# Performance work log

Measured on AMD Instinct MI355X. Metric: run time of the kernel, lower is better.

Reference implementation:

```python
import jax, jax.numpy as jnp
import numpy as np

M = 1024       # input feature dim
T_EXPERTS = 64 # number of experts
K = 2          # top-k
TOKENS = 65536 # B*N flattened tokens


def setup_inputs() -> dict:
    key = jax.random.key(0)
    ks = jax.random.split(key, 6)
    return {
        "x": jax.random.normal(ks[0], (TOKENS, M), dtype=jnp.float32),
        "noise": jax.random.normal(ks[1], (TOKENS, T_EXPERTS), dtype=jnp.float32),
        "Wg_w": jax.random.normal(ks[2], (T_EXPERTS, M), dtype=jnp.float32) * 0.02,
        "Wg_b": jax.random.normal(ks[3], (T_EXPERTS,), dtype=jnp.float32) * 0.02,
        "Wn_w": jax.random.normal(ks[4], (T_EXPERTS, M), dtype=jnp.float32) * 0.02,
        "Wn_b": jax.random.normal(ks[5], (T_EXPERTS,), dtype=jnp.float32) * 0.02,
    }


def reference(x, noise, Wg_w, Wg_b, Wn_w, Wn_b):
    # logits = Wg(x); noise_scale = softplus(Wnoise(x))
    logits = jnp.einsum("bm,tm->bt", x, Wg_w) + Wg_b          # [tokens, t]
    noise_scale = jax.nn.softplus(jnp.einsum("bm,tm->bt", x, Wn_w) + Wn_b)
    H = logits + noise * noise_scale                           # noisy logits
    topk_vals, topk_idx = jax.lax.top_k(H, K)                  # [tokens, k]
    topk_softmax = jax.nn.softmax(topk_vals, axis=-1)
    # scatter softmax weights into sparse [tokens, t] gate tensor
    rows = jnp.arange(H.shape[0])[:, None]
    gates = jnp.zeros_like(H).at[rows, topk_idx].set(topk_softmax)
    return (gates, H, topk_idx, noise_scale, logits)
```

## Files before the change

kernel.cpp:

```cpp
#include <hip/hip_runtime.h>
#include <math.h>

#define NTOK 65536
#define MDIM 1024
#define NE   64
#define TB   128
#define NKC  32
#define DELTA 5e-4f

typedef float f32x4  __attribute__((ext_vector_type(4)));
typedef short bf16x8 __attribute__((ext_vector_type(8)));
typedef unsigned int u32;

__device__ __forceinline__ unsigned short f32_to_bf16_rne(float f) {
    u32 u = __builtin_bit_cast(u32, f);
    u32 r = u + 0x7FFFu + ((u >> 16) & 1u);
    return (unsigned short)(r >> 16);
}
__device__ __forceinline__ float bf16_to_f32(unsigned short h) {
    u32 u = ((u32)h) << 16;
    return __builtin_bit_cast(float, u);
}
__device__ __forceinline__ void gll16(const void* g, void* l) {
    __builtin_amdgcn_global_load_lds(
        (const __attribute__((address_space(1))) u32*)g,
        (__attribute__((address_space(3))) u32*)l, 16, 0, 0);
}

__global__ __launch_bounds__(256) void split_w_kernel(
    const float* __restrict__ Wg_w, const float* __restrict__ Wn_w,
    unsigned short* __restrict__ ws, u32* __restrict__ cnt)
{
    if (blockIdx.x == 0 && threadIdx.x == 0) *cnt = 0;

    const int gid  = blockIdx.x * 256 + threadIdx.x;
    const int kc   = gid >> 10;
    const int rest = gid & 1023;
    const int tm   = rest >> 8;
    const int mat  = (rest >> 7) & 1;
    const int sp   = (rest >> 6) & 1;
    const int lane = rest & 63;
    const int e    = (lane & 15) + 16 * tm;
    const int k0   = kc * 32 + 8 * (lane >> 4);
    const float* W = mat ? Wn_w : Wg_w;

    unsigned short o[8];
#pragma unroll
    for (int i = 0; i < 8; ++i) {
        const float v = W[(size_t)e * MDIM + k0 + i];
        const u32 u  = __builtin_bit_cast(u32, v);
        const unsigned short hb = (unsigned short)(u >> 16);
        o[i] = sp ? f32_to_bf16_rne(v - bf16_to_f32(hb)) : hb;
    }
    uint4 pk;
    pk.x = (u32)o[0] | ((u32)o[1] << 16);
    pk.y = (u32)o[2] | ((u32)o[3] << 16);
    pk.z = (u32)o[4] | ((u32)o[5] << 16);
    pk.w = (u32)o[6] | ((u32)o[7] << 16);
    *reinterpret_cast<uint4*>(&ws[(size_t)gid * 8]) = pk;
}

__global__ __launch_bounds__(512, 4) void gate_mfma_kernel(
    const float* __restrict__ x,
    const float* __restrict__ noise,
    const unsigned short* __restrict__ ws,
    const float* __restrict__ Wg_b,
    const float* __restrict__ Wn_b,
    float* __restrict__ out_gates,
    float* __restrict__ out_H,
    float* __restrict__ out_idx,
    float* __restrict__ out_ns,
    float* __restrict__ out_logits,
    u32* __restrict__ cnt,
    u32* __restrict__ list)
{
    __shared__ unsigned short wbuf[2][8192];

    const int tid  = threadIdx.x;
    const int lane = tid & 63;
    const int w    = tid >> 6;
    const int c    = lane & 15;
    const int q    = lane >> 4;
    const int tokw = blockIdx.x * TB + w * 16;

    const float* __restrict__ xr = x + (size_t)(tokw + c) * MDIM + 8 * q;

    f32x4 acc[4][2];
#pragma unroll
    for (int tm = 0; tm < 4; ++tm)
#pragma unroll
        for (int m = 0; m < 2; ++m)
            acc[tm][m] = (f32x4){0.f, 0.f, 0.f, 0.f};

    gll16(ws + (size_t)tid * 8,         &wbuf[0][(size_t)tid * 8]);
    gll16(ws + (size_t)(tid + 512) * 8, &wbuf[0][(size_t)(tid + 512) * 8]);
    __builtin_amdgcn_sched_barrier(0);
    f32x4 xa = *reinterpret_cast<const f32x4*>(xr);
    f32x4 xb = *reinterpret_cast<const f32x4*>(xr + 4);
    __builtin_amdgcn_sched_barrier(0);
    asm volatile("s_waitcnt vmcnt(2)" ::: "memory");
    __syncthreads();

    int cur = 0;
    for (int kc = 0; kc < NKC; ++kc) {
        asm volatile("s_waitcnt vmcnt(0)" ::: "memory");

        bf16x8 xhi, xlo;
        {
            const float v[8] = {xa.x, xa.y, xa.z, xa.w, xb.x, xb.y, xb.z, xb.w};
            u32 hp[4], lp[4];
#pragma unroll
            for (int p = 0; p < 4; ++p) {
                const u32 u0 = __builtin_bit_cast(u32, v[2 * p]);
                const u32 u1 = __builtin_bit_cast(u32, v[2 * p + 1]);
                const float h0 = __builtin_bit_cast(float, u0 & 0xFFFF0000u);
                const float h1 = __builtin_bit_cast(float, u1 & 0xFFFF0000u);
                hp[p] = (u0 >> 16) | (u1 & 0xFFFF0000u);
                const u32 l0 = (u32)f32_to_bf16_rne(v[2 * p] - h0);
                const u32 l1 = (u32)f32_to_bf16_rne(v[2 * p + 1] - h1);
                lp[p] = l0 | (l1 << 16);
            }
            const uint4 h4 = {hp[0], hp[1], hp[2], hp[3]};
            const uint4 l4 = {lp[0], lp[1], lp[2], lp[3]};
            xhi = __builtin_bit_cast(bf16x8, h4);
            xlo = __builtin_bit_cast(bf16x8, l4);
        }

        if (kc + 1 < NKC) {
            const unsigned short* wc = ws + (size_t)(kc + 1) * 8192;
            gll16(wc + (size_t)tid * 8,         &wbuf[cur ^ 1][(size_t)tid * 8]);
            gll16(wc + (size_t)(tid + 512) * 8, &wbuf[cur ^ 1][(size_t)(tid + 512) * 8]);
            __builtin_amdgcn_sched_barrier(0);
            const int off = (kc + 1) * 32;
            xa = *reinterpret_cast<const f32x4*>(xr + off);
            xb = *reinterpret_cast<const f32x4*>(xr + off + 4);
            __builtin_amdgcn_sched_barrier(0);
        }

#pragma unroll
        for (int tm = 0; tm < 4; ++tm)
#pragma unroll
            for (int mat = 0; mat < 2; ++mat) {
                const int gbase = ((tm * 4 + mat * 2) * 64 + lane) * 8;
                const bf16x8 whi = *reinterpret_cast<const bf16x8*>(&wbuf[cur][gbase]);
                const bf16x8 wlo = *reinterpret_cast<const bf16x8*>(&wbuf[cur][gbase + 512]);
                f32x4 a = acc[tm][mat];
                a = __builtin_amdgcn_mfma_f32_16x16x32_bf16(wlo, xhi, a, 0, 0, 0);
                a = __builtin_amdgcn_mfma_f32_16x16x32_bf16(whi, xlo, a, 0, 0, 0);
                a = __builtin_amdgcn_mfma_f32_16x16x32_bf16(whi, xhi, a, 0, 0, 0);
                acc[tm][mat] = a;
            }

        if (kc + 1 < NKC) {
            asm volatile("s_waitcnt vmcnt(2)" ::: "memory");
            __syncthreads();
        }
        cur ^= 1;
    }

    f32x4 bgv[4], bnv[4];
#pragma unroll
    for (int tm = 0; tm < 4; ++tm) {
        bgv[tm] = *reinterpret_cast<const f32x4*>(&Wg_b[16 * tm + 4 * q]);
        bnv[tm] = *reinterpret_cast<const f32x4*>(&Wn_b[16 * tm + 4 * q]);
    }

    const int tok = tokw + c;
    float hv[4][4];

#pragma unroll
    for (int tm = 0; tm < 4; ++tm) {
        const size_t rb = (size_t)tok * NE + 16 * tm + 4 * q;
        const f32x4 nz = *reinterpret_cast<const f32x4*>(&noise[rb]);
        f32x4 lg, nsv, hh;
#pragma unroll
        for (int r = 0; r < 4; ++r) {
            lg[r] = acc[tm][0][r] + bgv[tm][r];
            const float nl = acc[tm][1][r] + bnv[tm][r];
            nsv[r] = fmaxf(nl, 0.f) + log1pf(expf(-fabsf(nl)));
            hh[r]  = fmaf(nz[r], nsv[r], lg[r]);
            hv[tm][r] = hh[r];
        }
        *reinterpret_cast<f32x4*>(&out_logits[rb]) = lg;
        *reinterpret_cast<f32x4*>(&out_ns[rb])     = nsv;
        *reinterpret_cast<f32x4*>(&out_H[rb])      = hh;
    }

    float v1 = -INFINITY, v2 = -INFINITY, v3 = -INFINITY;
    int   i1 = 0,         i2 = 0;
#pragma unroll
    for (int tm = 0; tm < 4; ++tm)
#pragma unroll
        for (int r = 0; r < 4; ++r) {
            const int ex = 16 * tm + 4 * q + r;
            const float hcur = hv[tm][r];
            if (hcur > v1)      { v3 = v2; v2 = v1; i2 = i1; v1 = hcur; i1 = ex; }
            else if (hcur > v2) { v3 = v2; v2 = hcur; i2 = ex; }
            else if (hcur > v3) { v3 = hcur; }
        }

#pragma unroll
    for (int off = 16; off <= 32; off <<= 1) {
        const float w1 = __shfl_xor(v1, off, 64);
        const int   k1 = __shfl_xor(i1, off, 64);
        const float w2 = __shfl_xor(v2, off, 64);
        const int   k2 = __shfl_xor(i2, off, 64);
        const float w3 = __shfl_xor(v3, off, 64);
        float m3;
        if (v1 >= w1) m3 = (v2 >= w1) ? fmaxf(v3, w1) : fmaxf(v2, w2);
        else          m3 = (w2 >= v1) ? fmaxf(w3, v1) : fmaxf(w2, v2);
        if (w1 > v1 || (w1 == v1 && k1 < i1)) {
            if (v1 > w2 || (v1 == w2 && i1 < k2)) { v2 = v1; i2 = i1; }
            else                                  { v2 = w2; i2 = k2; }
            v1 = w1; i1 = k1;
        } else {
            if (w1 > v2 || (w1 == v2 && k1 < i2)) { v2 = w1; i2 = k1; }
        }
        v3 = m3;
    }

    const float e2v = expf(v2 - v1);
    const float inv = 1.f / (1.f + e2v);
    const float p1  = inv;
    const float p2  = e2v * inv;

#pragma unroll
    for (int tm = 0; tm < 4; ++tm) {
        f32x4 g;
#pragma unroll
        for (int r = 0; r < 4; ++r) {
            const int ex = 16 * tm + 4 * q + r;
            g[r] = (ex == i1) ? p1 : ((ex == i2) ? p2 : 0.f);
        }
        *reinterpret_cast<f32x4*>(&out_gates[(size_t)tok * NE + 16 * tm + 4 * q]) = g;
    }
    if (q == 0) {
        *reinterpret_cast<float2*>(&out_idx[(size_t)tok * 2]) =
            make_float2((float)i1, (float)i2);
        if ((v1 - v2 < DELTA) || (v2 - v3 < DELTA)) {
            const u32 slot = atomicAdd(cnt, 1u);
            list[slot] = (u32)tok;
        }
    }
}

__global__ __launch_bounds__(64) void refine_kernel(
    const float* __restrict__ x,
    const float* __restrict__ noise,
    const float* __restrict__ Wg_w, const float* __restrict__ Wg_b,
    const float* __restrict__ Wn_w, const float* __restrict__ Wn_b,
    const u32* __restrict__ cnt, const u32* __restrict__ list,
    float* __restrict__ out_gates, float* __restrict__ out_idx)
{
    const int lane = threadIdx.x;
    const u32 n = *cnt;

    for (u32 it = blockIdx.x; it < n; it += gridDim.x) {
        const int tok = (int)list[it];

        f32x4 xv[4];
#pragma unroll
        for (int i = 0; i < 4; ++i)
            xv[i] = *reinterpret_cast<const f32x4*>(
                &x[(size_t)tok * MDIM + lane * 16 + i * 4]);

        float lgv = 0.f, nlv = 0.f;
        for (int e = 0; e < NE; ++e) {
            float sg = 0.f, sn = 0.f;
#pragma unroll
            for (int i = 0; i < 4; ++i) {
                const f32x4 wg = *reinterpret_cast<const f32x4*>(
                    &Wg_w[(size_t)e * MDIM + lane * 16 + i * 4]);
                const f32x4 wn = *reinterpret_cast<const f32x4*>(
                    &Wn_w[(size_t)e * MDIM + lane * 16 + i * 4]);
#pragma unroll
                for (int j = 0; j < 4; ++j) {
                    sg = fmaf(xv[i][j], wg[j], sg);
                    sn = fmaf(xv[i][j], wn[j], sn);
                }
            }
#pragma unroll
            for (int off = 32; off >= 1; off >>= 1) {
                sg += __shfl_xor(sg, off, 64);
                sn += __shfl_xor(sn, off, 64);
            }
            if (e == lane) { lgv = sg; nlv = sn; }
        }

        lgv += Wg_b[lane];
        nlv += Wn_b[lane];
        const float ns = fmaxf(nlv, 0.f) + log1pf(expf(-fabsf(nlv)));
        const float h  = fmaf(noise[(size_t)tok * NE + lane], ns, lgv);

        float v1 = h; int i1 = lane;
#pragma unroll
        for (int off = 32; off >= 1; off >>= 1) {
            const float ov = __shfl_xor(v1, off, 64);
            const int   oi = __shfl_xor(i1, off, 64);
            if (ov > v1 || (ov == v1 && oi < i1)) { v1 = ov; i1 = oi; }
        }
        float v2 = (lane == i1) ? -INFINITY : h; int i2 = lane;
#pragma unroll
        for (int off = 32; off >= 1; off >>= 1) {
            const float ov = __shfl_xor(v2, off, 64);
            const int   oi = __shfl_xor(i2, off, 64);
            if (ov > v2 || (ov == v2 && oi < i2)) { v2 = ov; i2 = oi; }
        }

        const float e2v = expf(v2 - v1);
        const float inv = 1.f / (1.f + e2v);
        const float p1  = inv;
        const float p2  = e2v * inv;

        out_gates[(size_t)tok * NE + lane] =
            (lane == i1) ? p1 : ((lane == i2) ? p2 : 0.f);
        if (lane == 0) {
            *reinterpret_cast<float2*>(&out_idx[(size_t)tok * 2]) =
                make_float2((float)i1, (float)i2);
        }
    }
}

extern "C" void kernel_launch(void* const* d_in, const int* in_sizes, int n_in,
                              void* d_out, int out_size, void* d_ws, size_t ws_size,
                              hipStream_t stream) {
    const float* x     = (const float*)d_in[0];
    const float* noise = (const float*)d_in[1];
    const float* Wg_w  = (const float*)d_in[2];
    const float* Wg_b  = (const float*)d_in[3];
    const float* Wn_w  = (const float*)d_in[4];
    const float* Wn_b  = (const float*)d_in[5];

    float* out = (float*)d_out;
    float* out_gates  = out;
    float* out_H      = out + (size_t)NTOK * NE;
    float* out_idx    = out + (size_t)2 * NTOK * NE;
    float* out_ns     = out + (size_t)2 * NTOK * NE + (size_t)NTOK * 2;
    float* out_logits = out + (size_t)3 * NTOK * NE + (size_t)NTOK * 2;

    unsigned short* wsplit = (unsigned short*)d_ws;
    u32* cnt  = (u32*)((char*)d_ws + 524288);
    u32* list = (u32*)((char*)d_ws + 524304);

    split_w_kernel<<<dim3(128), dim3(256), 0, stream>>>(Wg_w, Wn_w, wsplit, cnt);
    gate_mfma_kernel<<<dim3(NTOK / TB), dim3(512), 0, stream>>>(
        x, noise, wsplit, Wg_b, Wn_b,
        out_gates, out_H, out_idx, out_ns, out_logits, cnt, list);
    refine_kernel<<<dim3(1024), dim3(64), 0, stream>>>(
        x, noise, Wg_w, Wg_b, Wn_w, Wn_b, cnt, list, out_gates, out_idx);
}
```

Measured before the change: 143.6 us.

## Prefetch x two chunks ahead and stagger K-chunk start per block

Restructures the K loop so x is loaded in bursts of two chunks, held in a double-buffered register set two groups ahead, and the loop is fully unrolled. Each block starts its K traversal at a different chunk offset, derived from the block index, so concurrent blocks spread their weight-chunk reads. The loop now waits only on the weight loads and lets the x loads run deeper in flight, aiming to hide HBM latency for the memory-bound x stream. It costs more VGPRs for the extra x buffers and a larger unrolled code body, and changes the fp32 accumulation order.

```diff
diff --git a/kernel.cpp b/kernel.cpp
--- a/kernel.cpp
+++ b/kernel.cpp
@@ -82,6 +82,7 @@
     const int c    = lane & 15;
     const int q    = lane >> 4;
     const int tokw = blockIdx.x * TB + w * 16;
+    const int p    = (blockIdx.x & 15) * 2;
 
     const float* __restrict__ xr = x + (size_t)(tokw + c) * MDIM + 8 * q;
 
@@ -92,71 +93,101 @@
         for (int m = 0; m < 2; ++m)
             acc[tm][m] = (f32x4){0.f, 0.f, 0.f, 0.f};
 
-    gll16(ws + (size_t)tid * 8,         &wbuf[0][(size_t)tid * 8]);
-    gll16(ws + (size_t)(tid + 512) * 8, &wbuf[0][(size_t)(tid + 512) * 8]);
-    __builtin_amdgcn_sched_barrier(0);
-    f32x4 xa = *reinterpret_cast<const f32x4*>(xr);
-    f32x4 xb = *reinterpret_cast<const f32x4*>(xr + 4);
-    __builtin_amdgcn_sched_barrier(0);
-    asm volatile("s_waitcnt vmcnt(2)" ::: "memory");
+    f32x4 xs[2][2][2];
+
+#define XBURST(G, SET)                                                          \
+    {                                                                           \
+        const int cA_ = (p + 2 * (G)) & (NKC - 1);                              \
+        const int cB_ = (p + 2 * (G) + 1) & (NKC - 1);                          \
+        xs[SET][0][0] = *reinterpret_cast<const f32x4*>(xr + cA_ * 32);         \
+        xs[SET][0][1] = *reinterpret_cast<const f32x4*>(xr + cA_ * 32 + 4);     \
+        xs[SET][1][0] = *reinterpret_cast<const f32x4*>(xr + cB_ * 32);         \
+        xs[SET][1][1] = *reinterpret_cast<const f32x4*>(xr + cB_ * 32 + 4);     \
+        __builtin_amdgcn_sched_barrier(0);                                      \
+    }
+#define WGLL(CI, BUF)                                                           \
+    {                                                                           \
+        const unsigned short* wc_ = ws + (size_t)(CI) * 8192;                   \
+        gll16(wc_ + (size_t)tid * 8,         &wbuf[BUF][(size_t)tid * 8]);      \
+        gll16(wc_ + (size_t)(tid + 512) * 8, &wbuf[BUF][(size_t)(tid + 512) * 8]); \
+        __builtin_amdgcn_sched_barrier(0);                                      \
+    }
+
+    WGLL(p, 0)
+    XBURST(0, 0)
+    XBURST(1, 1)
+    asm volatile("s_waitcnt vmcnt(8)" ::: "memory");
     __syncthreads();
+    asm volatile("s_waitcnt vmcnt(4)" ::: "memory");
 
     int cur = 0;
-    for (int kc = 0; kc < NKC; ++kc) {
-        asm volatile("s_waitcnt vmcnt(0)" ::: "memory");
-
-        bf16x8 xhi, xlo;
-        {
-            const float v[8] = {xa.x, xa.y, xa.z, xa.w, xb.x, xb.y, xb.z, xb.w};
-            u32 hp[4], lp[4];
-#pragma unroll
-            for (int p = 0; p < 4; ++p) {
-                const u32 u0 = __builtin_bit_cast(u32, v[2 * p]);
-                const u32 u1 = __builtin_bit_cast(u32, v[2 * p + 1]);
-                const float h0 = __builtin_bit_cast(float, u0 & 0xFFFF0000u);
-                const float h1 = __builtin_bit_cast(float, u1 & 0xFFFF0000u);
-                hp[p] = (u0 >> 16) | (u1 & 0xFFFF0000u);
-                const u32 l0 = (u32)f32_to_bf16_rne(v[2 * p] - h0);
-                const u32 l1 = (u32)f32_to_bf16_rne(v[2 * p + 1] - h1);
-                lp[p] = l0 | (l1 << 16);
-            }
-            const uint4 h4 = {hp[0], hp[1], hp[2], hp[3]};
-            const uint4 l4 = {lp[0], lp[1], lp[2], lp[3]};
-            xhi = __builtin_bit_cast(bf16x8, h4);
-            xlo = __builtin_bit_cast(bf16x8, l4);
-        }
-
-        if (kc + 1 < NKC) {
-            const unsigned short* wc = ws + (size_t)(kc + 1) * 8192;
-            gll16(wc + (size_t)tid * 8,         &wbuf[cur ^ 1][(size_t)tid * 8]);
-            gll16(wc + (size_t)(tid + 512) * 8, &wbuf[cur ^ 1][(size_t)(tid + 512) * 8]);
+#pragma unroll
+    for (int g = 0; g < NKC / 2; ++g) {
+#pragma unroll
+        for (int j = 0; j < 2; ++j) {
+            const int i  = 2 * g + j;
+            const int st = g & 1;
+
+            bf16x8 xhi, xlo;
+            {
+                const f32x4 a = xs[st][j][0];
+                const f32x4 b = xs[st][j][1];
+                const float v[8] = {a.x, a.y, a.z, a.w, b.x, b.y, b.z, b.w};
+                u32 hp[4], lp[4];
+#pragma unroll
+                for (int pp = 0; pp < 4; ++pp) {
+                    const u32 u0 = __builtin_bit_cast(u32, v[2 * pp]);
+                    const u32 u1 = __builtin_bit_cast(u32, v[2 * pp + 1]);
+                    const float h0 = __builtin_bit_cast(float, u0 & 0xFFFF0000u);
+                    const float h1 = __builtin_bit_cast(float, u1 & 0xFFFF0000u);
+                    hp[pp] = (u0 >> 16) | (u1 & 0xFFFF0000u);
+                    const u32 l0 = (u32)f32_to_bf16_rne(v[2 * pp] - h0);
+                    const u32 l1 = (u32)f32_to_bf16_rne(v[2 * pp + 1] - h1);
+                    lp[pp] = l0 | (l1 << 16);
+                }
+                const uint4 h4 = {hp[0], hp[1], hp[2], hp[3]};
+                const uint4 l4 = {lp[0], lp[1], lp[2], lp[3]};
+                xhi = __builtin_bit_cast(bf16x8, h4);
+                xlo = __builtin_bit_cast(bf16x8, l4);
+            }
             __builtin_amdgcn_sched_barrier(0);
-            const int off = (kc + 1) * 32;
-            xa = *reinterpret_cast<const f32x4*>(xr + off);
-            xb = *reinterpret_cast<const f32x4*>(xr + off + 4);
-            __builtin_amdgcn_sched_barrier(0);
-        }
-
-#pragma unroll
-        for (int tm = 0; tm < 4; ++tm)
-#pragma unroll
-            for (int mat = 0; mat < 2; ++mat) {
-                const int gbase = ((tm * 4 + mat * 2) * 64 + lane) * 8;
-                const bf16x8 whi = *reinterpret_cast<const bf16x8*>(&wbuf[cur][gbase]);
-                const bf16x8 wlo = *reinterpret_cast<const bf16x8*>(&wbuf[cur][gbase + 512]);
-                f32x4 a = acc[tm][mat];
-                a = __builtin_amdgcn_mfma_f32_16x16x32_bf16(wlo, xhi, a, 0, 0, 0);
-                a = __builtin_amdgcn_mfma_f32_16x16x32_bf16(whi, xlo, a, 0, 0, 0);
-                a = __builtin_amdgcn_mfma_f32_16x16x32_bf16(whi, xhi, a, 0, 0, 0);
-                acc[tm][mat] = a;
-            }
-
-        if (kc + 1 < NKC) {
-            asm volatile("s_waitcnt vmcnt(2)" ::: "memory");
-            __syncthreads();
-        }
-        cur ^= 1;
-    }
+
+            const bool have_next = (i + 1 < NKC);
+            if (have_next) {
+                WGLL((p + i + 1) & (NKC - 1), cur ^ 1)
+            }
+            const bool burst = (j == 1) && (g + 2 < NKC / 2);
+            if (burst) {
+                XBURST(g + 2, st)
+            }
+
+#pragma unroll
+            for (int tm = 0; tm < 4; ++tm)
+#pragma unroll
+                for (int mat = 0; mat < 2; ++mat) {
+                    const int gbase = ((tm * 4 + mat * 2) * 64 + lane) * 8;
+                    const bf16x8 whi = *reinterpret_cast<const bf16x8*>(&wbuf[cur][gbase]);
+                    const bf16x8 wlo = *reinterpret_cast<const bf16x8*>(&wbuf[cur][gbase + 512]);
+                    f32x4 a = acc[tm][mat];
+                    a = __builtin_amdgcn_mfma_f32_16x16x32_bf16(wlo, xhi, a, 0, 0, 0);
+                    a = __builtin_amdgcn_mfma_f32_16x16x32_bf16(whi, xlo, a, 0, 0, 0);
+                    a = __builtin_amdgcn_mfma_f32_16x16x32_bf16(whi, xhi, a, 0, 0, 0);
+                    acc[tm][mat] = a;
+                }
+
+            if (have_next) {
+                if (burst) {
+                    asm volatile("s_waitcnt vmcnt(4)" ::: "memory");
+                } else {
+                    asm volatile("s_waitcnt vmcnt(0)" ::: "memory");
+                }
+                __syncthreads();
+                cur ^= 1;
+            }
+        }
+    }
+#undef XBURST
+#undef WGLL
 
     f32x4 bgv[4], bnv[4];
 #pragma unroll
```

After: 148.5 us. +3.4%, slower.
